# Kernel tuning notes

Measured on AMD Instinct MI355X. Metric: run time of the kernel, lower is better.

The kernel has to match this reference:

```python
import jax, jax.numpy as jnp
import numpy as np

NUM_HEADS = 16

def setup_inputs() -> dict:
    key = jax.random.key(0)
    ks = jax.random.split(key, 5)
    b, c, w, h = 2, 1024, 48, 48
    sc = 0.02
    return {
        "x": jax.random.normal(ks[0], (b, c, w, h), jnp.float32),
        "Wqkv": jax.random.normal(ks[1], (3 * c, c), jnp.float32) * sc,
        "bqkv": jax.random.normal(ks[2], (3 * c,), jnp.float32) * sc,
        "Wo": jax.random.normal(ks[3], (c, c), jnp.float32) * sc,
        "bo": jax.random.normal(ks[4], (c,), jnp.float32) * sc,
    }

def reference(x, Wqkv, bqkv, Wo, bo):
    b, c, w, h = x.shape
    n = NUM_HEADS
    hd = c // n
    s = w * h
    # [b,c,w,h] -> tokens [b, s, c]
    xs = x.transpose(0, 2, 3, 1).reshape(b, s, c)
    qkv = xs @ Wqkv.T + bqkv                       # [b, s, 3c]
    # rearrange 'b s (three n hd) -> three b n s hd'
    qkv = qkv.reshape(b, s, 3, n, hd).transpose(2, 0, 3, 1, 4)
    q, k, v = qkv[0], qkv[1], qkv[2]               # [b, n, s, hd]
    score = jnp.einsum('bnqh,bnkh->bnqk', q, k) / jnp.sqrt(jnp.float32(hd))
    # module uses a soft causal mask: subtract 10000 above the diagonal
    mask = 10000.0 * jnp.triu(jnp.ones((s, s), dtype=score.dtype), k=1)
    attn = jax.nn.softmax(score - mask, axis=-1)   # [b, n, s, s]
    z = jnp.einsum('bnqk,bnkh->bqnh', attn, v).reshape(b, s, c)
    out = z @ Wo.T + bo                            # [b, s, c]
    return out.reshape(b, w, h, c).transpose(0, 3, 1, 2)
```

## Files before the change

kernel.cpp:

```cpp
#include <hip/hip_runtime.h>

typedef __bf16 bf16;
typedef __bf16 bf16x8 __attribute__((ext_vector_type(8)));
typedef float floatx4 __attribute__((ext_vector_type(4)));
typedef float floatx16 __attribute__((ext_vector_type(16)));

static constexpr int S = 2304;
static constexpr int C = 1024;
static constexpr int NHEAD = 16;
static constexpr int HDIM = 64;
static constexpr int BATCH = 2;
static constexpr float QSCALE = 0.18033688011112042f;
static constexpr int QSPLIT = 12;
static constexpr int NACC = S - QSPLIT * 64;

__global__ __launch_bounds__(256) void k_zero(float4* __restrict__ p, int n4) {
  int i = blockIdx.x * 256 + threadIdx.x;
  if (i < n4) p[i] = float4{0.f, 0.f, 0.f, 0.f};
}

__global__ __launch_bounds__(256) void k_convert(const float* __restrict__ src,
                                                 bf16* __restrict__ dst, int n8) {
  int i = blockIdx.x * 256 + threadIdx.x;
  if (i >= n8) return;
  float4 a = *(const float4*)(src + (size_t)i * 8);
  float4 b = *(const float4*)(src + (size_t)i * 8 + 4);
  bf16x8 o;
  o[0] = (bf16)a.x; o[1] = (bf16)a.y; o[2] = (bf16)a.z; o[3] = (bf16)a.w;
  o[4] = (bf16)b.x; o[5] = (bf16)b.y; o[6] = (bf16)b.z; o[7] = (bf16)b.w;
  *(bf16x8*)(dst + (size_t)i * 8) = o;
}

__global__ __launch_bounds__(256) void k_transpose(const float* __restrict__ x,
                                                   bf16* __restrict__ xs) {
  __shared__ bf16 T[64 * 72];
  int c0 = blockIdx.x * 64, t0 = blockIdx.y * 64, b = blockIdx.z;
  int tid = threadIdx.x;
  const float* xb = x + (size_t)b * C * S;
#pragma unroll
  for (int it = 0; it < 4; ++it) {
    int idx = it * 256 + tid;
    int rc = idx >> 4, t4 = idx & 15;
    float4 v = *(const float4*)(xb + (size_t)(c0 + rc) * S + t0 + t4 * 4);
    T[(t4 * 4 + 0) * 72 + rc] = (bf16)v.x;
    T[(t4 * 4 + 1) * 72 + rc] = (bf16)v.y;
    T[(t4 * 4 + 2) * 72 + rc] = (bf16)v.z;
    T[(t4 * 4 + 3) * 72 + rc] = (bf16)v.w;
  }
  __syncthreads();
  bf16* xsb = xs + (size_t)b * S * C;
#pragma unroll
  for (int it = 0; it < 2; ++it) {
    int idx = it * 256 + tid;
    int rt = idx >> 3, c8 = idx & 7;
    bf16x8 v;
#pragma unroll
    for (int i = 0; i < 8; ++i) v[i] = T[rt * 72 + c8 * 8 + i];
    *(bf16x8*)(xsb + (size_t)(t0 + rt) * C + c0 + c8 * 8) = v;
  }
}

__device__ __forceinline__ void g2l16(const bf16* g, bf16* l) {
  __builtin_amdgcn_global_load_lds(
      (const __attribute__((address_space(1))) void*)g,
      (__attribute__((address_space(3))) void*)l, 16, 0, 0);
}

__device__ __forceinline__ unsigned cvtpk(float a, float b) {
  unsigned r;
  asm("v_cvt_pk_bf16_f32 %0, %1, %2" : "=v"(r) : "v"(a), "v"(b));
  return r;
}

__device__ __forceinline__ void pl32(unsigned& a, unsigned& b) {
  asm("v_permlane32_swap_b32 %0, %1" : "+v"(a), "+v"(b));
}

template <int EPI>
__global__ __launch_bounds__(256) void k_gemm_bt(const bf16* __restrict__ A,
                                                 const bf16* __restrict__ Bt,
                                                 const float* __restrict__ bias,
                                                 bf16* __restrict__ q,
                                                 bf16* __restrict__ k,
                                                 bf16* __restrict__ v,
                                                 float* __restrict__ outf) {
  constexpr int K = C;
  __shared__ bf16 As[128 * 64];
  __shared__ bf16 Bs[128 * 64];
  int tid = threadIdx.x;
  int w = tid >> 6, lane = tid & 63, ln = lane & 15, quad = lane >> 4;
  int m0 = blockIdx.y * 128, n0 = blockIdx.x * 128;
  int moff = (w >> 1) * 64, noff = (w & 1) * 64;
  floatx4 acc[4][4] = {};

  int sr[4], sc[4];
#pragma unroll
  for (int it = 0; it < 4; ++it) {
    int L = (it * 4 + w) * 64 + lane;
    sr[it] = L >> 3;
    sc[it] = (L & 7) ^ (sr[it] & 7);
  }

  for (int k0 = 0; k0 < K; k0 += 64) {
    __syncthreads();
#pragma unroll
    for (int it = 0; it < 4; ++it) {
      int cb = (it * 4 + w) * 64;
      g2l16(A + (size_t)(m0 + sr[it]) * K + k0 + sc[it] * 8, As + cb * 8);
      g2l16(Bt + (size_t)(n0 + sr[it]) * K + k0 + sc[it] * 8, Bs + cb * 8);
    }
    __syncthreads();
#pragma unroll
    for (int t = 0; t < 2; ++t) {
      bf16x8 af[4], bfr[4];
#pragma unroll
      for (int i = 0; i < 4; ++i) {
        int ra = moff + i * 16 + ln;
        af[i]  = *(const bf16x8*)(As + ra * 64 + (((t * 4 + quad) ^ (ra & 7))) * 8);
        int rb = noff + i * 16 + ln;
        bfr[i] = *(const bf16x8*)(Bs + rb * 64 + (((t * 4 + quad) ^ (rb & 7))) * 8);
      }
#pragma unroll
      for (int im = 0; im < 4; ++im)
#pragma unroll
        for (int in = 0; in < 4; ++in)
          acc[im][in] = __builtin_amdgcn_mfma_f32_16x16x32_bf16(
              af[im], bfr[in], acc[im][in], 0, 0, 0);
    }
  }

  int bidx = (m0 >= S) ? 1 : 0;
  if (EPI == 0) {
#pragma unroll
    for (int in = 0; in < 4; ++in) {
      int j = n0 + noff + in * 16 + ln;
      float bv = bias[j];
      int three = j >> 10;
      int head = (j >> 6) & 15;
      int hdi = j & 63;
#pragma unroll
      for (int im = 0; im < 4; ++im) {
        int mbase = m0 + moff + im * 16 + quad * 4;
        int tb = mbase - bidx * S;
        if (three == 2) {
          union { ushort4 u; bf16 h[4]; } P;
#pragma unroll
          for (int r = 0; r < 4; ++r) P.h[r] = (bf16)(acc[im][in][r] + bv);
          *(ushort4*)(v + ((size_t)(bidx * NHEAD + head) * HDIM + hdi) * S + tb) = P.u;
        } else if (three == 0) {
          bf16* dst = q + ((size_t)(bidx * NHEAD + head) * S + tb) * HDIM + hdi;
#pragma unroll
          for (int r = 0; r < 4; ++r)
            dst[(size_t)r * HDIM] = (bf16)((acc[im][in][r] + bv) * QSCALE);
        } else {
          bf16* dst = k + ((size_t)(bidx * NHEAD + head) * S + tb) * HDIM + hdi;
#pragma unroll
          for (int r = 0; r < 4; ++r) dst[(size_t)r * HDIM] = (bf16)(acc[im][in][r] + bv);
        }
      }
    }
  } else {
#pragma unroll
    for (int in = 0; in < 4; ++in) {
      int co = n0 + noff + in * 16 + ln;
      float bv = bias[co];
#pragma unroll
      for (int im = 0; im < 4; ++im) {
        int mbase = m0 + moff + im * 16 + quad * 4;
        int tb = mbase - bidx * S;
        float4 st;
        st.x = acc[im][in][0] + bv;
        st.y = acc[im][in][1] + bv;
        st.z = acc[im][in][2] + bv;
        st.w = acc[im][in][3] + bv;
        *(float4*)(outf + ((size_t)bidx * C + co) * S + tb) = st;
      }
    }
  }
}

__global__ __launch_bounds__(512) void k_attn_part(const bf16* __restrict__ Qg,
                                                   const bf16* __restrict__ Kg,
                                                   const bf16* __restrict__ Vtg,
                                                   bf16* __restrict__ z,
                                                   float* __restrict__ Oacc,
                                                   float* __restrict__ Lacc) {
  __shared__ bf16 Ks[2][64 * 64];
  __shared__ bf16 Vs[2][64 * 64];
  static const unsigned char QT[31] = {2,1,8,8,8,8,8,8,7,7,6,6,6,5,5,5,5,3,
                                       7,7,7,7,6,6,4,4,4,4,3,3,0};
  static const unsigned char LO[31] = {0,0,0,6,12,18,24,30,0,6,0,6,12,0,6,12,18,0,
                                       12,17,22,27,18,23,0,5,10,15,6,11,0};
  static const unsigned char HI[31] = {12,8,6,12,18,24,30,36,6,12,6,12,18,6,12,18,24,6,
                                       17,22,27,32,23,28,5,10,15,20,11,16,4};
  int i = blockIdx.x;
  int xcd = i & 7, j = i >> 3;
  int grp = j / 31, r = j % 31;
  int bh = xcd + 8 * grp;
  int qt = QT[r], lo = LO[r], hi = HI[r];
  bool single = (qt <= 2);
  int b = bh >> 4, h = bh & 15;
  int tid = threadIdx.x;
  int w = tid >> 6, lane = tid & 63;
  int ql = lane & 31, hw = lane >> 5;
  int qw = qt * 256 + w * 32;
  int qg = qw + ql;
  int ktd = qw >> 6;

  const bf16* kb = Kg + (size_t)bh * S * HDIM;
  const bf16* vb = Vtg + (size_t)bh * HDIM * S;

  int s_row = tid >> 3;
  int s_c8 = (tid & 7) ^ (s_row & 7);
  size_t kOff = (size_t)s_row * HDIM + s_c8 * 8;
  size_t vOff = (size_t)s_row * S + s_c8 * 8;

  const bf16* qb = Qg + ((size_t)bh * S + qg) * HDIM + hw * 8;
  bf16x8 qf[4];
#pragma unroll
  for (int c = 0; c < 4; ++c) qf[c] = *(const bf16x8*)(qb + c * 16);

  float lsA = 0.f, lsB = 0.f;
  floatx16 o0 = {}, o1 = {};

  const bf16* kb0 = kb + (size_t)lo * 64 * HDIM;
  const bf16* vb0 = vb + (size_t)lo * 64;
  g2l16(kb0 + kOff, Ks[0] + tid * 8);
  g2l16(vb0 + vOff, Vs[0] + tid * 8);

  const bf16* kbn = kb0 + (size_t)64 * HDIM;
  const bf16* vbn = vb0 + 64;

  int qsw = ql & 7;

#pragma unroll 1
  for (int kt = lo; kt < hi; ++kt) {
    int cur = (kt - lo) & 1;
    __syncthreads();

    if (kt + 1 < hi) {
      g2l16(kbn + kOff, Ks[1 - cur] + tid * 8);
      g2l16(vbn + vOff, Vs[1 - cur] + tid * 8);
      kbn += (size_t)64 * HDIM;
      vbn += 64;
    }

    if (kt > ktd) continue;
    bool diag = (kt == ktd);

    const bf16* ksb = Ks[cur];
    const bf16* vsb = Vs[cur];

    floatx16 sa0 = {}, sa1 = {};
    __builtin_amdgcn_s_setprio(1);
#pragma unroll
    for (int c = 0; c < 4; ++c) {
      int c8 = ((2 * c + hw) ^ qsw) * 8;
      bf16x8 k0 = *(const bf16x8*)(ksb + ql * 64 + c8);
      bf16x8 k1 = *(const bf16x8*)(ksb + (32 + ql) * 64 + c8);
      sa0 = __builtin_amdgcn_mfma_f32_32x32x16_bf16(k0, qf[c], sa0, 0, 0, 0);
      sa1 = __builtin_amdgcn_mfma_f32_32x32x16_bf16(k1, qf[c], sa1, 0, 0, 0);
    }
    __builtin_amdgcn_s_setprio(0);

    unsigned pk0[8], pk1[8];
    if (!diag) {
#pragma unroll
      for (int t = 0; t < 8; ++t) {
        float a = exp2f(sa0[2 * t]), c2 = exp2f(sa0[2 * t + 1]);
        float d = exp2f(sa1[2 * t]), e = exp2f(sa1[2 * t + 1]);
        lsA += a + c2;
        lsB += d + e;
        pk0[t] = cvtpk(a, c2);
        pk1[t] = cvtpk(d, e);
      }
    } else {
      int qd = qg - kt * 64;
#pragma unroll
      for (int t = 0; t < 8; ++t) {
        int r0 = 2 * t, r1 = 2 * t + 1;
        int k0l = (r0 & 3) + 8 * (r0 >> 2) + 4 * hw;
        int k1l = (r1 & 3) + 8 * (r1 >> 2) + 4 * hw;
        float a = (k0l > qd) ? 0.f : exp2f(sa0[r0]);
        float c2 = (k1l > qd) ? 0.f : exp2f(sa0[r1]);
        float d = (32 + k0l > qd) ? 0.f : exp2f(sa1[r0]);
        float e = (32 + k1l > qd) ? 0.f : exp2f(sa1[r1]);
        lsA += a + c2;
        lsB += d + e;
        pk0[t] = cvtpk(a, c2);
        pk1[t] = cvtpk(d, e);
      }
    }

    __builtin_amdgcn_s_setprio(1);
#pragma unroll
    for (int ktc = 0; ktc < 4; ++ktc) {
      unsigned d0, d1, d2, d3;
      if (ktc == 0)      { d0 = pk0[0]; d1 = pk0[1]; d2 = pk0[2]; d3 = pk0[3]; }
      else if (ktc == 1) { d0 = pk0[4]; d1 = pk0[5]; d2 = pk0[6]; d3 = pk0[7]; }
      else if (ktc == 2) { d0 = pk1[0]; d1 = pk1[1]; d2 = pk1[2]; d3 = pk1[3]; }
      else               { d0 = pk1[4]; d1 = pk1[5]; d2 = pk1[6]; d3 = pk1[7]; }
      pl32(d0, d2);
      pl32(d1, d3);
      union { unsigned u[4]; bf16x8 v; } pf;
      pf.u[0] = d0; pf.u[1] = d1; pf.u[2] = d2; pf.u[3] = d3;
      int c8 = ((2 * ktc + hw) ^ qsw) * 8;
      bf16x8 v0 = *(const bf16x8*)(vsb + ql * 64 + c8);
      bf16x8 v1 = *(const bf16x8*)(vsb + (32 + ql) * 64 + c8);
      o0 = __builtin_amdgcn_mfma_f32_32x32x16_bf16(v0, pf.v, o0, 0, 0, 0);
      o1 = __builtin_amdgcn_mfma_f32_32x32x16_bf16(v1, pf.v, o1, 0, 0, 0);
    }
    __builtin_amdgcn_s_setprio(0);
  }

  float lsum = lsA + lsB;
  lsum += __shfl_xor(lsum, 32);

  if (single) {
    float inv = 1.f / lsum;
    bf16* dst = z + ((size_t)b * S + qg) * C + h * HDIM + 4 * hw;
#pragma unroll
    for (int hdblk = 0; hdblk < 2; ++hdblk) {
#pragma unroll
      for (int rg = 0; rg < 4; ++rg) {
        union { ushort4 u; bf16 hh[4]; } P;
#pragma unroll
        for (int jj = 0; jj < 4; ++jj) {
          float ov = hdblk ? o1[rg * 4 + jj] : o0[rg * 4 + jj];
          P.hh[jj] = (bf16)(ov * inv);
        }
        *(ushort4*)(dst + hdblk * 32 + rg * 8) = P.u;
      }
    }
  } else {
    int qa = qg - QSPLIT * 64;
    if (hw == 0) atomicAdd(&Lacc[bh * NACC + qa], lsum);
#pragma unroll
    for (int hdblk = 0; hdblk < 2; ++hdblk) {
#pragma unroll
      for (int rr = 0; rr < 16; ++rr) {
        int hd = hdblk * 32 + (rr & 3) + 8 * (rr >> 2) + 4 * hw;
        float ov = hdblk ? o1[rr] : o0[rr];
        atomicAdd(&Oacc[((size_t)bh * 64 + hd) * NACC + qa], ov);
      }
    }
  }
}

__global__ __launch_bounds__(256) void k_norm(const float* __restrict__ Oacc,
                                              const float* __restrict__ Lacc,
                                              bf16* __restrict__ z) {
  __shared__ float T[64 * 65];
  int qt = blockIdx.x, bh = blockIdx.y;
  int b = bh >> 4, h = bh & 15;
  int qrel0 = qt * 64;
  int q0 = QSPLIT * 64 + qrel0;
  int tid = threadIdx.x;
  int q4 = (tid & 15) * 4, hd0 = tid >> 4;
  float4 lv = *(const float4*)(Lacc + bh * NACC + qrel0 + q4);
  float inv0 = 1.f / lv.x, inv1 = 1.f / lv.y, inv2 = 1.f / lv.z, inv3 = 1.f / lv.w;
#pragma unroll
  for (int hf = 0; hf < 4; ++hf) {
    int hd = hf * 16 + hd0;
    float4 v = *(const float4*)(Oacc + ((size_t)bh * 64 + hd) * NACC + qrel0 + q4);
    T[(q4 + 0) * 65 + hd] = v.x * inv0;
    T[(q4 + 1) * 65 + hd] = v.y * inv1;
    T[(q4 + 2) * 65 + hd] = v.z * inv2;
    T[(q4 + 3) * 65 + hd] = v.w * inv3;
  }
  __syncthreads();
#pragma unroll
  for (int it = 0; it < 2; ++it) {
    int idx = it * 256 + tid;
    int qq = idx >> 3, c8 = idx & 7;
    bf16x8 o;
#pragma unroll
    for (int k = 0; k < 8; ++k) o[k] = (bf16)T[qq * 65 + c8 * 8 + k];
    *(bf16x8*)(z + ((size_t)b * S + q0 + qq) * C + h * HDIM + c8 * 8) = o;
  }
}

extern "C" void kernel_launch(void* const* d_in, const int* in_sizes, int n_in,
                              void* d_out, int out_size, void* d_ws, size_t ws_size,
                              hipStream_t stream) {
  const float* x    = (const float*)d_in[0];
  const float* Wqkv = (const float*)d_in[1];
  const float* bqkv = (const float*)d_in[2];
  const float* Wo   = (const float*)d_in[3];
  const float* bo   = (const float*)d_in[4];
  float* out = (float*)d_out;

  bf16* ws = (bf16*)d_ws;
  const size_t tok = (size_t)BATCH * S * C;
  bf16* xs   = ws;
  bf16* Qg   = ws + tok;
  bf16* Kg   = ws + 2 * tok;
  bf16* Vtg  = ws + 3 * tok;
  bf16* Wqb  = ws + 4 * tok;
  bf16* Wob  = Wqb + (size_t)3 * C * C;
  float* Oacc = (float*)(Wob + (size_t)C * C);
  float* Lacc = Oacc + (size_t)32 * 64 * NACC;
  bf16* z    = xs;

  k_zero<<<3120, 256, 0, stream>>>((float4*)Oacc, 798720);
  k_convert<<<(3 * C * C / 8 + 255) / 256, 256, 0, stream>>>(Wqkv, Wqb, 3 * C * C / 8);
  k_convert<<<(C * C / 8 + 255) / 256, 256, 0, stream>>>(Wo, Wob, C * C / 8);
  k_transpose<<<dim3(C / 64, S / 64, BATCH), 256, 0, stream>>>(x, xs);
  k_gemm_bt<0><<<dim3(3 * C / 128, BATCH * S / 128), 256, 0, stream>>>(
      xs, Wqb, bqkv, Qg, Kg, Vtg, nullptr);
  k_attn_part<<<dim3(992), 512, 0, stream>>>(Qg, Kg, Vtg, z, Oacc, Lacc);
  k_norm<<<dim3(24, 32), 256, 0, stream>>>(Oacc, Lacc, z);
  k_gemm_bt<1><<<dim3(C / 128, BATCH * S / 128), 256, 0, stream>>>(
      z, Wob, bo, nullptr, nullptr, nullptr, out);
}
```

Measured before the change: 229.2 us.

## Replace atomic split-K attention accumulation with fixed two-way partial buffers

Rebalances the causal attention work schedule so that long query tiles are split into exactly two KV-range partitions, and short tiles run in a single pass. The old variable split used float atomics plus a zeroing kernel. Each partition now writes its O and l partials to its own buffer with plain vector stores, and the normalization kernel sums the two partials. This removes the zero-fill launch and the atomic traffic. In exchange the grid is smaller (512 blocks), the load balance per block may be less even, and the partial buffers are larger.

```diff
diff --git a/kernel.cpp b/kernel.cpp
--- a/kernel.cpp
+++ b/kernel.cpp
@@ -11,13 +11,9 @@
 static constexpr int HDIM = 64;
 static constexpr int BATCH = 2;
 static constexpr float QSCALE = 0.18033688011112042f;
-static constexpr int QSPLIT = 12;
-static constexpr int NACC = S - QSPLIT * 64;
-
-__global__ __launch_bounds__(256) void k_zero(float4* __restrict__ p, int n4) {
-  int i = blockIdx.x * 256 + threadIdx.x;
-  if (i < n4) p[i] = float4{0.f, 0.f, 0.f, 0.f};
-}
+static constexpr int QACC0 = 512;
+static constexpr int NACCQ = S - QACC0;
+static constexpr int NPART = 2;
 
 __global__ __launch_bounds__(256) void k_convert(const float* __restrict__ src,
                                                  bf16* __restrict__ dst, int n8) {
@@ -187,18 +183,16 @@
                                                    float* __restrict__ Lacc) {
   __shared__ bf16 Ks[2][64 * 64];
   __shared__ bf16 Vs[2][64 * 64];
-  static const unsigned char QT[31] = {2,1,8,8,8,8,8,8,7,7,6,6,6,5,5,5,5,3,
-                                       7,7,7,7,6,6,4,4,4,4,3,3,0};
-  static const unsigned char LO[31] = {0,0,0,6,12,18,24,30,0,6,0,6,12,0,6,12,18,0,
-                                       12,17,22,27,18,23,0,5,10,15,6,11,0};
-  static const unsigned char HI[31] = {12,8,6,12,18,24,30,36,6,12,6,12,18,6,12,18,24,6,
-                                       17,22,27,32,23,28,5,10,15,20,11,16,4};
+  static const unsigned char QT[16] = {8,8,7,7,6,6,5,5,4,4,1,3,3,2,2,0};
+  static const unsigned char LO[16] = {0,18,0,16,0,14,0,12,0,10,0,0,8,0,6,0};
+  static const unsigned char HI[16] = {18,36,16,32,14,28,12,24,10,20,8,8,16,6,12,4};
+  static const unsigned char PT[16] = {0,1,0,1,0,1,0,1,0,1,0,0,1,0,1,0};
   int i = blockIdx.x;
   int xcd = i & 7, j = i >> 3;
-  int grp = j / 31, r = j % 31;
+  int grp = j >> 4, r = j & 15;
   int bh = xcd + 8 * grp;
-  int qt = QT[r], lo = LO[r], hi = HI[r];
-  bool single = (qt <= 2);
+  int qt = QT[r], lo = LO[r], hi = HI[r], part = PT[r];
+  bool single = (qt <= 1);
   int b = bh >> 4, h = bh & 15;
   int tid = threadIdx.x;
   int w = tid >> 6, lane = tid & 63;
@@ -333,16 +327,15 @@
       }
     }
   } else {
-    int qa = qg - QSPLIT * 64;
-    if (hw == 0) atomicAdd(&Lacc[bh * NACC + qa], lsum);
-#pragma unroll
-    for (int hdblk = 0; hdblk < 2; ++hdblk) {
-#pragma unroll
-      for (int rr = 0; rr < 16; ++rr) {
-        int hd = hdblk * 32 + (rr & 3) + 8 * (rr >> 2) + 4 * hw;
-        float ov = hdblk ? o1[rr] : o0[rr];
-        atomicAdd(&Oacc[((size_t)bh * 64 + hd) * NACC + qa], ov);
-      }
+    int qa = qg - QACC0;
+    float* ob = Oacc + (((size_t)part * 32 + bh) * NACCQ + qa) * 64;
+    if (hw == 0) Lacc[((size_t)part * 32 + bh) * NACCQ + qa] = lsum;
+#pragma unroll
+    for (int g = 0; g < 4; ++g) {
+      *(float4*)(ob + 4 * hw + 8 * g) =
+          float4{o0[4 * g], o0[4 * g + 1], o0[4 * g + 2], o0[4 * g + 3]};
+      *(float4*)(ob + 32 + 4 * hw + 8 * g) =
+          float4{o1[4 * g], o1[4 * g + 1], o1[4 * g + 2], o1[4 * g + 3]};
     }
   }
 }
@@ -350,33 +343,34 @@
 __global__ __launch_bounds__(256) void k_norm(const float* __restrict__ Oacc,
                                               const float* __restrict__ Lacc,
                                               bf16* __restrict__ z) {
-  __shared__ float T[64 * 65];
   int qt = blockIdx.x, bh = blockIdx.y;
   int b = bh >> 4, h = bh & 15;
-  int qrel0 = qt * 64;
-  int q0 = QSPLIT * 64 + qrel0;
   int tid = threadIdx.x;
-  int q4 = (tid & 15) * 4, hd0 = tid >> 4;
-  float4 lv = *(const float4*)(Lacc + bh * NACC + qrel0 + q4);
-  float inv0 = 1.f / lv.x, inv1 = 1.f / lv.y, inv2 = 1.f / lv.z, inv3 = 1.f / lv.w;
-#pragma unroll
-  for (int hf = 0; hf < 4; ++hf) {
-    int hd = hf * 16 + hd0;
-    float4 v = *(const float4*)(Oacc + ((size_t)bh * 64 + hd) * NACC + qrel0 + q4);
-    T[(q4 + 0) * 65 + hd] = v.x * inv0;
-    T[(q4 + 1) * 65 + hd] = v.y * inv1;
-    T[(q4 + 2) * 65 + hd] = v.z * inv2;
-    T[(q4 + 3) * 65 + hd] = v.w * inv3;
-  }
-  __syncthreads();
-#pragma unroll
-  for (int it = 0; it < 2; ++it) {
-    int idx = it * 256 + tid;
-    int qq = idx >> 3, c8 = idx & 7;
+  int q = tid >> 2;
+  int seg = tid & 3;
+  int qa = qt * 64 + q;
+  float l = Lacc[(size_t)bh * NACCQ + qa] +
+            Lacc[((size_t)32 + bh) * NACCQ + qa];
+  float inv = 1.f / l;
+  const float* o0 = Oacc + ((size_t)bh * NACCQ + qa) * 64 + seg * 16;
+  const float* o1 = Oacc + (((size_t)32 + bh) * NACCQ + qa) * 64 + seg * 16;
+  bf16* dst = z + ((size_t)b * S + QACC0 + qa) * C + h * HDIM + seg * 16;
+#pragma unroll
+  for (int half = 0; half < 2; ++half) {
+    float4 a0 = *(const float4*)(o0 + half * 8);
+    float4 a1 = *(const float4*)(o0 + half * 8 + 4);
+    float4 b0 = *(const float4*)(o1 + half * 8);
+    float4 b1 = *(const float4*)(o1 + half * 8 + 4);
     bf16x8 o;
-#pragma unroll
-    for (int k = 0; k < 8; ++k) o[k] = (bf16)T[qq * 65 + c8 * 8 + k];
-    *(bf16x8*)(z + ((size_t)b * S + q0 + qq) * C + h * HDIM + c8 * 8) = o;
+    o[0] = (bf16)((a0.x + b0.x) * inv);
+    o[1] = (bf16)((a0.y + b0.y) * inv);
+    o[2] = (bf16)((a0.z + b0.z) * inv);
+    o[3] = (bf16)((a0.w + b0.w) * inv);
+    o[4] = (bf16)((a1.x + b1.x) * inv);
+    o[5] = (bf16)((a1.y + b1.y) * inv);
+    o[6] = (bf16)((a1.z + b1.z) * inv);
+    o[7] = (bf16)((a1.w + b1.w) * inv);
+    *(bf16x8*)(dst + half * 8) = o;
   }
 }
 
@@ -399,17 +393,16 @@
   bf16* Wqb  = ws + 4 * tok;
   bf16* Wob  = Wqb + (size_t)3 * C * C;
   float* Oacc = (float*)(Wob + (size_t)C * C);
-  float* Lacc = Oacc + (size_t)32 * 64 * NACC;
+  float* Lacc = Oacc + (size_t)NPART * 32 * NACCQ * 64;
   bf16* z    = xs;
 
-  k_zero<<<3120, 256, 0, stream>>>((float4*)Oacc, 798720);
   k_convert<<<(3 * C * C / 8 + 255) / 256, 256, 0, stream>>>(Wqkv, Wqb, 3 * C * C / 8);
   k_convert<<<(C * C / 8 + 255) / 256, 256, 0, stream>>>(Wo, Wob, C * C / 8);
   k_transpose<<<dim3(C / 64, S / 64, BATCH), 256, 0, stream>>>(x, xs);
   k_gemm_bt<0><<<dim3(3 * C / 128, BATCH * S / 128), 256, 0, stream>>>(
       xs, Wqb, bqkv, Qg, Kg, Vtg, nullptr);
-  k_attn_part<<<dim3(992), 512, 0, stream>>>(Qg, Kg, Vtg, z, Oacc, Lacc);
-  k_norm<<<dim3(24, 32), 256, 0, stream>>>(Oacc, Lacc, z);
+  k_attn_part<<<dim3(512), 512, 0, stream>>>(Qg, Kg, Vtg, z, Oacc, Lacc);
+  k_norm<<<dim3(28, 32), 256, 0, stream>>>(Oacc, Lacc, z);
   k_gemm_bt<1><<<dim3(C / 128, BATCH * S / 128), 256, 0, stream>>>(
       z, Wob, bo, nullptr, nullptr, nullptr, out);
 }
```

Result: faster. 223.1 us (-2.7%).
